# Optimization experiments

Hardware: AMD Instinct MI355X
Metric: run time of the kernel (lower is better)

## Reference

```python
import jax, jax.numpy as jnp
import numpy as np

N, E = 20000, 320000
IN_DIM, EDGE_DIM, HID = 64, 16, 64
# (in_c, heads, channels, out_c) per layer; last layer heads=1, concat=False
DIMS = [(64, 4, 64, 256), (256, 4, 64, 256), (256, 1, 64, 64)]


def _ln(x, g, b):
    m = x.mean(-1, keepdims=True)
    v = x.var(-1, keepdims=True)
    return (x - m) / jnp.sqrt(v + 1e-5) * g + b


def _gatv2(x, ei, ea, Wl, bl, Wr, br, We, att, bc, concat):
    # PyG GATv2Conv, eval mode (no dropout), add_self_loops=True, fill_value='mean'
    n = x.shape[0]
    H, C = att.shape
    ar = jnp.arange(n, dtype=ei.dtype)
    src = jnp.concatenate([ei[0], ar])
    dst = jnp.concatenate([ei[1], ar])
    ea_f = jnp.concatenate([ea, jnp.broadcast_to(ea.mean(0), (n, ea.shape[1]))], 0)
    xl = (x @ Wl + bl).reshape(n, H, C)   # source transform
    xr = (x @ Wr + br).reshape(n, H, C)   # target transform
    ee = (ea_f @ We).reshape(-1, H, C)    # edge transform (no bias in PyG)
    e = jax.nn.leaky_relu(xl[src] + xr[dst] + ee, 0.2)       # [E+N, H, C]
    score = jnp.einsum('ehc,hc->eh', e, att)                 # [E+N, H]
    mx = jax.ops.segment_max(score, dst, num_segments=n)
    a = jnp.exp(score - mx[dst])
    a = a / (jax.ops.segment_sum(a, dst, num_segments=n)[dst] + 1e-16)
    out = jax.ops.segment_sum(a[:, :, None] * xl[src], dst, num_segments=n)  # [N,H,C]
    out = out.reshape(n, H * C) if concat else out.mean(1)
    return out + bc


def _forward(x, eis, eas, Wp, bp, gp, bep, layers):
    h = jax.nn.gelu(_ln(x @ Wp + bp, gp, bep), approximate=False)
    for i in range(3):
        Wl, bl, Wr, br, We, att, bc, g, be, Wsk, bsk = layers[i]
        res = h @ Wsk + bsk
        h = _gatv2(h, eis[i], eas[i], Wl, bl, Wr, br, We, att, bc, i < 2)
        h = jax.nn.gelu(_ln(h, g, be), approximate=False) + res
    return h


def setup_inputs() -> dict:
    key = jax.random.key(0)
    ks = iter(jax.random.split(key, 64))
    rn = lambda shape, s=0.05: jax.random.normal(next(ks), shape, jnp.float32) * s
    d = {'x': jax.random.normal(next(ks), (N, IN_DIM), jnp.float32)}
    for i in range(3):
        d['ei%d' % i] = jax.random.randint(next(ks), (2, E), 0, N, jnp.int32)
        d['ea%d' % i] = jax.random.normal(next(ks), (E, EDGE_DIM), jnp.float32)
    d['Wp'] = rn((IN_DIM, HID)); d['bp'] = jnp.zeros(HID)
    d['gp'] = jnp.ones(HID); d['bep'] = jnp.zeros(HID)
    for i, (ic, H, C, oc) in enumerate(DIMS):
        hc = H * C
        d['Wl%d' % i] = rn((ic, hc)); d['bl%d' % i] = jnp.zeros(hc)
        d['Wr%d' % i] = rn((ic, hc)); d['br%d' % i] = jnp.zeros(hc)
        d['We%d' % i] = rn((EDGE_DIM, hc))
        d['att%d' % i] = rn((H, C), 0.1)
        d['bc%d' % i] = jnp.zeros(hc if i < 2 else C)
        d['g%d' % i] = jnp.ones(oc); d['be%d' % i] = jnp.zeros(oc)
        d['Wsk%d' % i] = rn((ic, oc)); d['bsk%d' % i] = jnp.zeros(oc)
    return d


def reference(x, ei0, ea0, ei1, ea1, ei2, ea2, Wp, bp, gp, bep,
              Wl0, bl0, Wr0, br0, We0, att0, bc0, g0, be0, Wsk0, bsk0,
              Wl1, bl1, Wr1, br1, We1, att1, bc1, g1, be1, Wsk1, bsk1,
              Wl2, bl2, Wr2, br2, We2, att2, bc2, g2, be2, Wsk2, bsk2):
    layers = [
        (Wl0, bl0, Wr0, br0, We0, att0, bc0, g0, be0, Wsk0, bsk0),
        (Wl1, bl1, Wr1, br1, We1, att1, bc1, g1, be1, Wsk1, bsk1),
        (Wl2, bl2, Wr2, br2, We2, att2, bc2, g2, be2, Wsk2, bsk2),
    ]
    return _forward(x, (ei0, ei1, ei2), (ea0, ea1, ea2), Wp, bp, gp, bep, layers)
```

## Files before the change

kernel.cpp:

```cpp
#include <hip/hip_runtime.h>
#include <hip/hip_bf16.h>
#include <math.h>

#define NV 20000
#define NE 320000
#define CSR_PAD 8

typedef __attribute__((ext_vector_type(8))) short bf16x8;
typedef __attribute__((ext_vector_type(4))) float f32x4;
typedef __attribute__((ext_vector_type(2))) _Float16 h2;

static __device__ __forceinline__ ushort f2b(float f) {
  __hip_bfloat16 h = __float2bfloat16(f);
  return *reinterpret_cast<ushort*>(&h);
}
static __device__ __forceinline__ float b2f(ushort u) {
  union { ushort s[2]; float f; } c;
  c.s[0] = 0; c.s[1] = u;
  return c.f;
}
static __device__ __forceinline__ ushort f2h(float f) {
  _Float16 h = (_Float16)f;
  return *reinterpret_cast<ushort*>(&h);
}
static __device__ __forceinline__ float blo(unsigned u) { return __uint_as_float(u << 16); }
static __device__ __forceinline__ float bhi(unsigned u) { return __uint_as_float(u & 0xffff0000u); }

static __device__ __forceinline__ float wave_sum64(float x) {
  x += __int_as_float(__builtin_amdgcn_update_dpp(0, __float_as_int(x), 0x111, 0xF, 0xF, true));
  x += __int_as_float(__builtin_amdgcn_update_dpp(0, __float_as_int(x), 0x112, 0xF, 0xF, true));
  x += __int_as_float(__builtin_amdgcn_update_dpp(0, __float_as_int(x), 0x114, 0xF, 0xF, true));
  x += __int_as_float(__builtin_amdgcn_update_dpp(0, __float_as_int(x), 0x118, 0xF, 0xF, true));
  x += __int_as_float(__builtin_amdgcn_update_dpp(0, __float_as_int(x), 0x142, 0xA, 0xF, true));
  x += __int_as_float(__builtin_amdgcn_update_dpp(0, __float_as_int(x), 0x143, 0xC, 0xF, true));
  return __int_as_float(__builtin_amdgcn_readlane(__float_as_int(x), 63));
}

static __device__ __forceinline__ float sum16(float x) {
  x += __int_as_float(__builtin_amdgcn_update_dpp(0, __float_as_int(x), 0x121, 0xF, 0xF, true));
  x += __int_as_float(__builtin_amdgcn_update_dpp(0, __float_as_int(x), 0x122, 0xF, 0xF, true));
  x += __int_as_float(__builtin_amdgcn_update_dpp(0, __float_as_int(x), 0x124, 0xF, 0xF, true));
  x += __int_as_float(__builtin_amdgcn_update_dpp(0, __float_as_int(x), 0x128, 0xF, 0xF, true));
  return x;
}

static __device__ __forceinline__ float dot16h(const uint4* __restrict__ E,
                                               const h2* __restrict__ Wch) {
#if __has_builtin(__builtin_amdgcn_fdot2)
  const h2* e = (const h2*)E;
  float s = 0.f;
#pragma unroll
  for (int j = 0; j < 8; ++j) s = __builtin_amdgcn_fdot2(e[j], Wch[j], s, false);
  return s;
#else
  const unsigned* u = (const unsigned*)E;
  float s = 0.f;
#pragma unroll
  for (int j = 0; j < 8; ++j) {
    union { unsigned v; h2 h; } cv; cv.v = u[j];
    s = fmaf((float)cv.h[0], (float)Wch[j][0], s);
    s = fmaf((float)cv.h[1], (float)Wch[j][1], s);
  }
  return s;
#endif
}

struct CJob { const float* src; ushort* dst; int K, M; };
struct PrepArgs {
  const int* ei[3];
  const float* ea[3];
  int* counts[3];
  float* easum[3];
  CJob jobs[9];
  const float *x, *Wp, *bp, *gp, *bep;
  ushort* h0;
};

__global__ __launch_bounds__(256) void prep_kernel(PrepArgs a) {
  const int y = blockIdx.y, t = threadIdx.x;
  if (y < 3) {
    if (blockIdx.x < 256) {
      const float4* ea4 = (const float4*)a.ea[y];
      const int cg = t & 3;
      int r = blockIdx.x * 64 + (t >> 2);
      const int rstride = 256 * 64;
      float4 s = make_float4(0.f, 0.f, 0.f, 0.f);
      for (; r < NE; r += rstride) {
        float4 v = ea4[(size_t)r * 4 + cg];
        s.x += v.x; s.y += v.y; s.z += v.z; s.w += v.w;
      }
      __shared__ float4 red4[256];
      red4[t] = s;
      __syncthreads();
      if (t < 4) {
        float4 tot = make_float4(0.f, 0.f, 0.f, 0.f);
        for (int j = t; j < 256; j += 4) {
          float4 v = red4[j];
          tot.x += v.x; tot.y += v.y; tot.z += v.z; tot.w += v.w;
        }
        atomicAdd(&a.easum[y][t * 4 + 0], tot.x);
        atomicAdd(&a.easum[y][t * 4 + 1], tot.y);
        atomicAdd(&a.easum[y][t * 4 + 2], tot.z);
        atomicAdd(&a.easum[y][t * 4 + 3], tot.w);
      }
    }
    int i = blockIdx.x * 256 + t;
    if (i < NE) atomicAdd(&a.counts[y][a.ei[y][NE + i]], 1);
  } else if (y == 3) {
#pragma unroll
    for (int j = 0; j < 9; ++j) {
      CJob jb = a.jobs[j];
      const int total = jb.M * jb.K;
      for (int i = blockIdx.x * 256 + t; i < total; i += gridDim.x * 256) {
        int m = i / jb.K, k = i - m * jb.K;
        jb.dst[i] = f2b(jb.src[(size_t)k * jb.M + m]);
      }
    }
  } else {
    int wid = t >> 6, lane = t & 63;
    for (int row = blockIdx.x * 4 + wid; row < NV; row += gridDim.x * 4) {
      float xv = a.x[(size_t)row * 64 + lane];
      float acc = a.bp[lane];
#pragma unroll
      for (int k = 0; k < 64; ++k) {
        float v = __shfl(xv, k, 64);
        acc = fmaf(v, a.Wp[k * 64 + lane], acc);
      }
      float s1 = wave_sum64(acc), s2 = wave_sum64(acc * acc);
      float mean = s1 * (1.0f / 64.0f);
      float var  = s2 * (1.0f / 64.0f) - mean * mean;
      float yv = (acc - mean) * rsqrtf(var + 1e-5f) * a.gp[lane] + a.bep[lane];
      float gel = 0.5f * yv * (1.0f + erff(yv * 0.70710678118654752f));
      a.h0[(size_t)row * 64 + lane] = f2b(gel);
    }
  }
}

__global__ __launch_bounds__(1024) void scan_kernel(
    int* __restrict__ countsA, int* __restrict__ cursorA)
{
  int* counts = countsA + blockIdx.x * (NV + 1);
  int* cursor = cursorA + blockIdx.x * NV;
  __shared__ int ws[16];
  __shared__ int wexcl[17];
  const int t = threadIdx.x, lane = t & 63, wid = t >> 6;
  const int base = t * 20;
  int v[20];
  int tot = 0;
#pragma unroll
  for (int j = 0; j < 20; ++j) {
    int i = base + j;
    v[j] = (i < NV) ? counts[i] : 0;
    tot += v[j];
  }
  int x = tot;
#pragma unroll
  for (int o = 1; o < 64; o <<= 1) {
    int yy = __shfl_up(x, o, 64);
    if (lane >= o) x += yy;
  }
  if (lane == 63) ws[wid] = x;
  __syncthreads();
  if (t == 0) {
    int r = 0;
#pragma unroll
    for (int j = 0; j < 16; ++j) { wexcl[j] = r; r += ws[j]; }
    wexcl[16] = r;
  }
  __syncthreads();
  int run = wexcl[wid] + (x - tot);
#pragma unroll
  for (int j = 0; j < 20; ++j) {
    int i = base + j;
    if (i < NV) { counts[i] = run; cursor[i] = run; }
    run += v[j];
  }
  if (t == 0) counts[NV] = wexcl[16];
}

struct G0SArgs {
  const ushort *A, *WT;
  const float *b0, *b1, *b2;
  ushort *O0, *O1; float* O2;
  int K, M1, M2, Mtot, NT;
  const int* ei[3]; const float* ea[3];
  int* cursor;
  unsigned* csr[3]; ushort* eab[3]; int HC[3];
};

__global__ __launch_bounds__(256) void gemm0_scatter_kernel(G0SArgs a) {
  __shared__ ushort As[128][40];
  __shared__ ushort Bs[64][40];
  const int t = threadIdx.x;
  if ((int)blockIdx.x < a.NT) {
    const int wave = t >> 6, lane = t & 63;
    const int mcols = a.Mtot >> 6;
    const int col0 = ((int)blockIdx.x % mcols) * 64, row0 = ((int)blockIdx.x / mcols) * 128;
    const int m_ = lane & 15, q = lane >> 4;
    f32x4 acc[2][4];
#pragma unroll
    for (int i = 0; i < 2; ++i)
#pragma unroll
      for (int j = 0; j < 4; ++j) acc[i][j] = (f32x4){0.f, 0.f, 0.f, 0.f};
    const int ar = t >> 1, ac = (t & 1) * 16;
    const int br = t >> 2, bcol = (t & 3) * 8;
    const ushort* Ap = a.A + (size_t)(row0 + ar) * a.K + ac;
    const ushort* Bp = a.WT + (size_t)(col0 + br) * a.K + bcol;
    const bool a_ok = (row0 + ar) < NV;
    for (int k0 = 0; k0 < a.K; k0 += 32) {
      uint4 av0 = make_uint4(0, 0, 0, 0), av1 = make_uint4(0, 0, 0, 0);
      if (a_ok) { av0 = *(const uint4*)(Ap + k0); av1 = *(const uint4*)(Ap + k0 + 8); }
      uint4 bv = *(const uint4*)(Bp + k0);
      *(uint4*)&As[ar][ac] = av0;
      *(uint4*)&As[ar][ac + 8] = av1;
      *(uint4*)&Bs[br][bcol] = bv;
      __syncthreads();
      bf16x8 a0 = *(const bf16x8*)&As[wave * 32 + m_][q * 8];
      bf16x8 a1 = *(const bf16x8*)&As[wave * 32 + 16 + m_][q * 8];
#pragma unroll
      for (int cf = 0; cf < 4; ++cf) {
        bf16x8 b = *(const bf16x8*)&Bs[cf * 16 + m_][q * 8];
        acc[0][cf] = __builtin_amdgcn_mfma_f32_16x16x32_bf16(a0, b, acc[0][cf], 0, 0, 0);
        acc[1][cf] = __builtin_amdgcn_mfma_f32_16x16x32_bf16(a1, b, acc[1][cf], 0, 0, 0);
      }
      __syncthreads();
    }
    const float* bias; int base, mode, Wd;
    if (col0 < a.M1)      { bias = a.b0; base = 0;    mode = 0; Wd = a.M1; }
    else if (col0 < a.M2) { bias = a.b1; base = a.M1; mode = 1; Wd = a.M2 - a.M1; }
    else                  { bias = a.b2; base = a.M2; mode = 2; Wd = a.Mtot - a.M2; }
#pragma unroll
    for (int rf = 0; rf < 2; ++rf) {
#pragma unroll
      for (int cf = 0; cf < 4; ++cf) {
        int col = col0 + cf * 16 + m_ - base;
        float bb = bias[col];
#pragma unroll
        for (int r = 0; r < 4; ++r) {
          int row = row0 + wave * 32 + rf * 16 + q * 4 + r;
          if (row < NV) {
            float v = acc[rf][cf][r] + bb;
            if (mode == 0)      a.O0[(size_t)row * Wd + col] = f2b(v);
            else if (mode == 1) a.O1[(size_t)row * Wd + col] = f2b(v);
            else                a.O2[(size_t)row * Wd + col] = v;
          }
        }
      }
    }
  } else {
    const int per = NE + CSR_PAD;
    int gi = ((int)blockIdx.x - a.NT) * 256 + t;
    if (gi >= 3 * per) return;
    int l = gi / per, i = gi - l * per;
    if (i >= NE) {
      a.csr[l][i] = 0u;
      uint4 z = make_uint4(0, 0, 0, 0);
      *(uint4*)(a.eab[l] + (size_t)i * 16) = z;
      *(uint4*)(a.eab[l] + (size_t)i * 16 + 8) = z;
      return;
    }
    int dst = a.ei[l][NE + i], src = a.ei[l][i];
    int pos = atomicAdd(&a.cursor[(size_t)l * NV + dst], 1);
    a.csr[l][pos] = (unsigned)(src * a.HC[l]);
    const float4* er = (const float4*)(a.ea[l] + (size_t)i * 16);
    float4 q0 = er[0], q1 = er[1], q2 = er[2], q3 = er[3];
    uint4 w0, w1;
    w0.x = (unsigned)f2h(q0.x) | ((unsigned)f2h(q0.y) << 16);
    w0.y = (unsigned)f2h(q0.z) | ((unsigned)f2h(q0.w) << 16);
    w0.z = (unsigned)f2h(q1.x) | ((unsigned)f2h(q1.y) << 16);
    w0.w = (unsigned)f2h(q1.z) | ((unsigned)f2h(q1.w) << 16);
    w1.x = (unsigned)f2h(q2.x) | ((unsigned)f2h(q2.y) << 16);
    w1.y = (unsigned)f2h(q2.z) | ((unsigned)f2h(q2.w) << 16);
    w1.z = (unsigned)f2h(q3.x) | ((unsigned)f2h(q3.y) << 16);
    w1.w = (unsigned)f2h(q3.z) | ((unsigned)f2h(q3.w) << 16);
    *(uint4*)(a.eab[l] + (size_t)pos * 16) = w0;
    *(uint4*)(a.eab[l] + (size_t)pos * 16 + 8) = w1;
  }
}

__global__ __launch_bounds__(256) void gemm_fused(
    const ushort* __restrict__ A, const ushort* __restrict__ WT,
    const float* __restrict__ b0, const float* __restrict__ b1,
    const float* __restrict__ b2,
    ushort* __restrict__ O0, ushort* __restrict__ O1, float* __restrict__ O2,
    int N, int K, int M1, int M2, int Mtot)
{
  __shared__ ushort As[128][40];
  __shared__ ushort Bs[64][40];
  const int t = threadIdx.x, wave = t >> 6, lane = t & 63;
  const int row0 = blockIdx.y * 128, col0 = blockIdx.x * 64;
  const int m_ = lane & 15, q = lane >> 4;
  f32x4 acc[2][4];
#pragma unroll
  for (int i = 0; i < 2; ++i)
#pragma unroll
    for (int j = 0; j < 4; ++j) acc[i][j] = (f32x4){0.f, 0.f, 0.f, 0.f};
  const int ar = t >> 1, ac = (t & 1) * 16;
  const int br = t >> 2, bcol = (t & 3) * 8;
  const ushort* Ap = A + (size_t)(row0 + ar) * K + ac;
  const ushort* Bp = WT + (size_t)(col0 + br) * K + bcol;
  const bool a_ok = (row0 + ar) < N;
  for (int k0 = 0; k0 < K; k0 += 32) {
    uint4 av0 = make_uint4(0, 0, 0, 0), av1 = make_uint4(0, 0, 0, 0);
    if (a_ok) { av0 = *(const uint4*)(Ap + k0); av1 = *(const uint4*)(Ap + k0 + 8); }
    uint4 bv = *(const uint4*)(Bp + k0);
    *(uint4*)&As[ar][ac] = av0;
    *(uint4*)&As[ar][ac + 8] = av1;
    *(uint4*)&Bs[br][bcol] = bv;
    __syncthreads();
    bf16x8 a0 = *(const bf16x8*)&As[wave * 32 + m_][q * 8];
    bf16x8 a1 = *(const bf16x8*)&As[wave * 32 + 16 + m_][q * 8];
#pragma unroll
    for (int cf = 0; cf < 4; ++cf) {
      bf16x8 b = *(const bf16x8*)&Bs[cf * 16 + m_][q * 8];
      acc[0][cf] = __builtin_amdgcn_mfma_f32_16x16x32_bf16(a0, b, acc[0][cf], 0, 0, 0);
      acc[1][cf] = __builtin_amdgcn_mfma_f32_16x16x32_bf16(a1, b, acc[1][cf], 0, 0, 0);
    }
    __syncthreads();
  }
  const float* bias; int base, mode, Wd;
  if (col0 < M1)      { bias = b0; base = 0;  mode = 0; Wd = M1; }
  else if (col0 < M2) { bias = b1; base = M1; mode = 1; Wd = M2 - M1; }
  else                { bias = b2; base = M2; mode = 2; Wd = Mtot - M2; }
#pragma unroll
  for (int rf = 0; rf < 2; ++rf) {
#pragma unroll
    for (int cf = 0; cf < 4; ++cf) {
      int col = col0 + cf * 16 + m_ - base;
      float bb = bias[col];
#pragma unroll
      for (int r = 0; r < 4; ++r) {
        int row = row0 + wave * 32 + rf * 16 + q * 4 + r;
        if (row < N) {
          float v = acc[rf][cf][r] + bb;
          if (mode == 0)      O0[(size_t)row * Wd + col] = f2b(v);
          else if (mode == 1) O1[(size_t)row * Wd + col] = f2b(v);
          else                O2[(size_t)row * Wd + col] = v;
        }
      }
    }
  }
}

__global__ __launch_bounds__(256) void agg4_kernel(
    const ushort* __restrict__ eab, const float* __restrict__ easum,
    const float* __restrict__ We,
    const ushort* __restrict__ xl, const ushort* __restrict__ xr,
    const float* __restrict__ att, const float* __restrict__ bc,
    const float* __restrict__ g, const float* __restrict__ be,
    const float* __restrict__ res,
    const int* __restrict__ offs, const unsigned* __restrict__ csr,
    ushort* __restrict__ houtb, int E)
{
  const int t = threadIdx.x, lane = t & 63, wave = t >> 6;
  const int n = blockIdx.x * 4 + wave;
  const int cb = 4 * lane;
  const size_t rowb = (size_t)n * 256 + cb;
  const float L2E = 1.4426950408889634f;

  float4 atv = *(const float4*)(att + cb);
  float at[4] = {atv.x * L2E, atv.y * L2E, atv.z * L2E, atv.w * L2E};

  h2 Wch[4][8];
  float esf[4] = {0.f, 0.f, 0.f, 0.f};
#pragma unroll
  for (int k = 0; k < 8; ++k) {
    float4 wr0 = *(const float4*)(We + (2 * k) * 256 + cb);
    float4 wr1 = *(const float4*)(We + (2 * k + 1) * 256 + cb);
    const float* w0 = &wr0.x;
    const float* w1 = &wr1.x;
    float e0 = easum[2 * k], e1 = easum[2 * k + 1];
#pragma unroll
    for (int j = 0; j < 4; ++j) {
      esf[j] = fmaf(e0, w0[j], esf[j]);
      esf[j] = fmaf(e1, w1[j], esf[j]);
      Wch[j][k] = (h2){(_Float16)w0[j], (_Float16)w1[j]};
    }
  }
#pragma unroll
  for (int j = 0; j < 4; ++j) esf[j] *= 1.0f / (float)E;

  uint2 qr = *(const uint2*)(xr + rowb);
  float xrv[4] = {blo(qr.x), bhi(qr.x), blo(qr.y), bhi(qr.y)};
  uint2 qn = *(const uint2*)(xl + rowb);
  float xln[4] = {blo(qn.x), bhi(qn.x), blo(qn.y), bhi(qn.y)};

  float p = 0.f;
#pragma unroll
  for (int j = 0; j < 4; ++j) {
    float v = xln[j] + xrv[j] + esf[j];
    v = v > 0.f ? v : 0.2f * v;
    p = fmaf(v, at[j], p);
  }
  float wself = exp2f(sum16(p));
  float acc[4];
#pragma unroll
  for (int j = 0; j < 4; ++j) acc[j] = wself * xln[j];
  float denom = wself;

  const int beg = __builtin_amdgcn_readfirstlane(offs[n]);
  const int end = __builtin_amdgcn_readfirstlane(offs[n + 1]);

  unsigned P[2];
  uint4 EA[2][2];
  uint2 XL[2];
#pragma unroll
  for (int k = 0; k < 2; ++k) {
    P[k] = csr[beg + k];
    const uint4* ep = (const uint4*)(eab + (size_t)(beg + k) * 16);
    EA[k][0] = ep[0]; EA[k][1] = ep[1];
  }
#pragma unroll
  for (int k = 0; k < 2; ++k)
    XL[k] = *(const uint2*)(xl + __builtin_amdgcn_readfirstlane(P[k]) + cb);

  for (int idx = beg; idx < end; idx += 2) {
    unsigned Q[2];
    uint4 EB[2][2];
    uint2 XN[2];
#pragma unroll
    for (int k = 0; k < 2; ++k) Q[k] = csr[idx + 2 + k];
#pragma unroll
    for (int k = 0; k < 2; ++k) {
      const uint4* ep = (const uint4*)(eab + (size_t)(idx + 2 + k) * 16);
      EB[k][0] = ep[0]; EB[k][1] = ep[1];
    }
#pragma unroll
    for (int k = 0; k < 2; ++k)
      XN[k] = *(const uint2*)(xl + __builtin_amdgcn_readfirstlane(Q[k]) + cb);

#pragma unroll
    for (int k = 0; k < 2; ++k) {
      float xf[4] = {blo(XL[k].x), bhi(XL[k].x), blo(XL[k].y), bhi(XL[k].y)};
      float pp = 0.f;
#pragma unroll
      for (int j = 0; j < 4; ++j) {
        float ee = dot16h(EA[k], Wch[j]);
        float v = xf[j] + xrv[j] + ee;
        v = v > 0.f ? v : 0.2f * v;
        pp = fmaf(v, at[j], pp);
      }
      float S = sum16(pp);
      float w = (idx + k < end) ? exp2f(S) : 0.f;
#pragma unroll
      for (int j = 0; j < 4; ++j) acc[j] = fmaf(w, xf[j], acc[j]);
      denom += w;
    }
#pragma unroll
    for (int k = 0; k < 2; ++k) { P[k] = Q[k]; EA[k][0] = EB[k][0]; EA[k][1] = EB[k][1]; XL[k] = XN[k]; }
  }

  const float inv = 1.0f / (denom + 1e-16f);
  float4 bcv = *(const float4*)(bc + cb);
  float out[4];
  out[0] = acc[0] * inv + bcv.x; out[1] = acc[1] * inv + bcv.y;
  out[2] = acc[2] * inv + bcv.z; out[3] = acc[3] * inv + bcv.w;

  float so1 = out[0] + out[1] + out[2] + out[3];
  float so2 = out[0] * out[0] + out[1] * out[1] + out[2] * out[2] + out[3] * out[3];
  float s1 = wave_sum64(so1), s2 = wave_sum64(so2);
  float mean = s1 * (1.0f / 256.0f);
  float var  = s2 * (1.0f / 256.0f) - mean * mean;
  float rstd = rsqrtf(var + 1e-5f);
  float4 gv = *(const float4*)(g + cb);
  float4 bev = *(const float4*)(be + cb);
  float4 rv = *(const float4*)(res + rowb);
  const float* gp = &gv.x; const float* bep = &bev.x; const float* rp = &rv.x;
  ushort ob[4];
#pragma unroll
  for (int j = 0; j < 4; ++j) {
    float y = (out[j] - mean) * rstd * gp[j] + bep[j];
    float gel = 0.5f * y * (1.0f + erff(y * 0.70710678118654752f));
    ob[j] = f2b(gel + rp[j]);
  }
  uint2 ov;
  ov.x = (unsigned)ob[0] | ((unsigned)ob[1] << 16);
  ov.y = (unsigned)ob[2] | ((unsigned)ob[3] << 16);
  *(uint2*)(houtb + rowb) = ov;
}

__global__ __launch_bounds__(256, 4) void agg1_kernel(
    const ushort* __restrict__ eab, const float* __restrict__ easum,
    const float* __restrict__ We,
    const ushort* __restrict__ xl, const ushort* __restrict__ xr,
    const float* __restrict__ att, const float* __restrict__ bc,
    const float* __restrict__ g, const float* __restrict__ be,
    const float* __restrict__ res,
    const int* __restrict__ offs, const unsigned* __restrict__ csr,
    float* __restrict__ houtf, int E)
{
  const int HC = 64;
  const int t = threadIdx.x, lane = t & 63, wave = t >> 6;
  const int n = blockIdx.x * 4 + wave;
  const int c = lane;

  const float xr_t = b2f(xr[(size_t)n * HC + c]);
  const float att_t = att[c] * 1.4426950408889634f;
  float eself = 0.f;
  h2 Wch[8];
#pragma unroll
  for (int j = 0; j < 8; ++j) {
    float w0 = We[(2 * j) * HC + c], w1 = We[(2 * j + 1) * HC + c];
    eself = fmaf(easum[2 * j], w0, eself);
    eself = fmaf(easum[2 * j + 1], w1, eself);
    Wch[j] = (h2){(_Float16)w0, (_Float16)w1};
  }
  eself *= 1.0f / (float)E;

  const float xln = b2f(xl[(size_t)n * HC + c]);
  float vs = xln + xr_t + eself;
  vs = vs > 0.f ? vs : 0.2f * vs;
  const float wself = exp2f(wave_sum64(vs * att_t));
  float acc = wself * xln, denom = wself;

  const int beg = __builtin_amdgcn_readfirstlane(offs[n]);
  const int end = __builtin_amdgcn_readfirstlane(offs[n + 1]);

  unsigned P[4];
  uint4 EA[4][2];
  float XL[4];
#pragma unroll
  for (int k = 0; k < 4; ++k) {
    P[k] = csr[beg + k];
    const uint4* ep = (const uint4*)(eab + (size_t)(beg + k) * 16);
    EA[k][0] = ep[0]; EA[k][1] = ep[1];
  }
#pragma unroll
  for (int k = 0; k < 4; ++k)
    XL[k] = b2f(xl[__builtin_amdgcn_readfirstlane(P[k]) + c]);

  for (int idx = beg; idx < end; idx += 4) {
    unsigned Q[4];
    uint4 EB[4][2];
    float XLN[4];
#pragma unroll
    for (int k = 0; k < 4; ++k) Q[k] = csr[idx + 4 + k];
#pragma unroll
    for (int k = 0; k < 4; ++k) {
      const uint4* ep = (const uint4*)(eab + (size_t)(idx + 4 + k) * 16);
      EB[k][0] = ep[0]; EB[k][1] = ep[1];
    }
#pragma unroll
    for (int k = 0; k < 4; ++k)
      XLN[k] = b2f(xl[__builtin_amdgcn_readfirstlane(Q[k]) + c]);

    float wv[4];
#pragma unroll
    for (int k = 0; k < 4; ++k) {
      float ee = dot16h(EA[k], Wch);
      float v = XL[k] + xr_t + ee;
      v = v > 0.f ? v : 0.2f * v;
      float S = wave_sum64(v * att_t);
      wv[k] = (idx + k < end) ? exp2f(S) : 0.f;
    }
#pragma unroll
    for (int k = 0; k < 4; ++k) { acc = fmaf(wv[k], XL[k], acc); denom += wv[k]; }
#pragma unroll
    for (int k = 0; k < 4; ++k) {
      P[k] = Q[k]; EA[k][0] = EB[k][0]; EA[k][1] = EB[k][1]; XL[k] = XLN[k];
    }
  }

  float out = acc / (denom + 1e-16f) + bc[c];
  float s1 = wave_sum64(out), s2 = wave_sum64(out * out);
  float mean = s1 / (float)HC;
  float var  = s2 / (float)HC - mean * mean;
  float y = (out - mean) * rsqrtf(var + 1e-5f) * g[c] + be[c];
  float gel = 0.5f * y * (1.0f + erff(y * 0.70710678118654752f));
  houtf[(size_t)n * HC + c] = gel + res[(size_t)n * HC + c];
}

extern "C" void kernel_launch(void* const* d_in, const int* in_sizes, int n_in,
                              void* d_out, int out_size, void* d_ws, size_t ws_size,
                              hipStream_t stream)
{
  auto in = [&](int i) { return (const float*)d_in[i]; };

  const int ic[3] = {64, 256, 256}, hc[3] = {256, 256, 64}, oc[3] = {256, 256, 64};
  const int CSRN = NE + CSR_PAD;

  char* w = (char*)d_ws;
  size_t off = 0;
  auto alloc = [&](size_t bytes) { void* p = w + off; off = (off + bytes + 511) & ~(size_t)511; return p; };
  ushort* B1   = (ushort*)alloc((size_t)NV * 256 * 2);
  ushort* B2   = (ushort*)alloc((size_t)NV * 256 * 2);
  float*  B3   = (float*)alloc((size_t)NV * 256 * 4);
  ushort* h0bf = (ushort*)alloc((size_t)NV * 64 * 2);
  ushort* h1bf = (ushort*)alloc((size_t)NV * 256 * 2);
  ushort* h2bf = (ushort*)alloc((size_t)NV * 256 * 2);
  ushort* Wcat[3];
  for (int i = 0; i < 3; ++i)
    Wcat[i] = (ushort*)alloc((size_t)(2 * hc[i] + oc[i]) * ic[i] * 2);
  float*    easumA  = (float*)alloc(3 * 64);
  int*      countsA = (int*)alloc((size_t)3 * (NV + 1) * 4);
  int*      cursorA = (int*)alloc((size_t)3 * NV * 4);
  unsigned* csrA    = (unsigned*)alloc((size_t)3 * CSRN * 4);
  ushort*   eabA    = (ushort*)alloc((size_t)3 * CSRN * 16 * 2);

  hipMemsetAsync(easumA, 0, 512 + (size_t)3 * (NV + 1) * 4, stream);

  PrepArgs pa;
  for (int i = 0; i < 3; ++i) {
    pa.ei[i] = (const int*)d_in[1 + 2 * i];
    pa.ea[i] = in(2 + 2 * i);
    pa.counts[i] = countsA + i * (NV + 1);
    pa.easum[i] = easumA + i * 16;
    pa.jobs[i * 3 + 0] = {in(11 + 11 * i), Wcat[i],                             ic[i], hc[i]};
    pa.jobs[i * 3 + 1] = {in(13 + 11 * i), Wcat[i] + (size_t)hc[i] * ic[i],     ic[i], hc[i]};
    pa.jobs[i * 3 + 2] = {in(20 + 11 * i), Wcat[i] + (size_t)2 * hc[i] * ic[i], ic[i], oc[i]};
  }
  pa.x = in(0); pa.Wp = in(7); pa.bp = in(8); pa.gp = in(9); pa.bep = in(10);
  pa.h0 = h0bf;
  prep_kernel<<<dim3(1344, 5), 256, 0, stream>>>(pa);

  scan_kernel<<<3, 1024, 0, stream>>>(countsA, cursorA);

  G0SArgs ga;
  ga.A = h0bf; ga.WT = Wcat[0];
  ga.b0 = in(12); ga.b1 = in(14); ga.b2 = in(21);
  ga.O0 = B1; ga.O1 = B2; ga.O2 = B3;
  ga.K = 64; ga.M1 = 256; ga.M2 = 512; ga.Mtot = 768;
  ga.NT = (768 / 64) * ((NV + 127) / 128);
  for (int i = 0; i < 3; ++i) {
    ga.ei[i] = (const int*)d_in[1 + 2 * i];
    ga.ea[i] = in(2 + 2 * i);
    ga.csr[i] = csrA + (size_t)i * CSRN;
    ga.eab[i] = eabA + (size_t)i * CSRN * 16;
    ga.HC[i] = hc[i];
  }
  ga.cursor = cursorA;
  const int scat_blocks = (3 * (NE + CSR_PAD) + 255) / 256;
  gemm0_scatter_kernel<<<ga.NT + scat_blocks, 256, 0, stream>>>(ga);

  agg4_kernel<<<NV / 4, 256, 0, stream>>>(
      eabA + 0, easumA + 0, in(15), B1, B2, in(16), in(17), in(18), in(19),
      B3, countsA, csrA, h1bf, NE);

  gemm_fused<<<dim3(768 / 64, (NV + 127) / 128), 256, 0, stream>>>(
      h1bf, Wcat[1], in(23), in(25), in(32), B1, B2, B3, NV, 256, 256, 512, 768);

  agg4_kernel<<<NV / 4, 256, 0, stream>>>(
      eabA + (size_t)CSRN * 16, easumA + 16, in(26), B1, B2, in(27), in(28),
      in(29), in(30), B3, countsA + (NV + 1), csrA + (size_t)CSRN, h2bf, NE);

  gemm_fused<<<dim3(192 / 64, (NV + 127) / 128), 256, 0, stream>>>(
      h2bf, Wcat[2], in(34), in(36), in(43), B1, B2, B3, NV, 256, 64, 128, 192);

  agg1_kernel<<<NV / 4, 256, 0, stream>>>(
      eabA + (size_t)2 * CSRN * 16, easumA + 32, in(37), B1, B2, in(38), in(39),
      in(40), in(41), B3, countsA + 2 * (NV + 1), csrA + (size_t)2 * CSRN,
      (float*)d_out, NE);
}
```

Before: 538.7 us.

## Store edge attrs in original order and index them via CSR pairs

The fp16 conversion of edge attributes moves into the prep kernel, which already streams the edge attributes for the mean. It writes them in original edge order instead of scattering them into CSR order. The CSR entries become (source offset, edge-attr offset) pairs, so the scatter pass writes 8 bytes per edge instead of 36. The aggregation kernels then gather edge attributes indirectly, in random order, instead of reading them sequentially, which trades coalesced reads in three aggregation passes for a cheaper build step. Padding entries point to edge 0, whose weight is masked anyway.

```diff
diff --git a/kernel.cpp b/kernel.cpp
--- a/kernel.cpp
+++ b/kernel.cpp
@@ -71,6 +71,7 @@
   const float* ea[3];
   int* counts[3];
   float* easum[3];
+  ushort* eab[3];
   CJob jobs[9];
   const float *x, *Wp, *bp, *gp, *bep;
   ushort* h0;
@@ -81,6 +82,7 @@
   if (y < 3) {
     if (blockIdx.x < 256) {
       const float4* ea4 = (const float4*)a.ea[y];
+      ushort* eab = a.eab[y];
       const int cg = t & 3;
       int r = blockIdx.x * 64 + (t >> 2);
       const int rstride = 256 * 64;
@@ -88,6 +90,10 @@
       for (; r < NE; r += rstride) {
         float4 v = ea4[(size_t)r * 4 + cg];
         s.x += v.x; s.y += v.y; s.z += v.z; s.w += v.w;
+        uint2 pk;
+        pk.x = (unsigned)f2h(v.x) | ((unsigned)f2h(v.y) << 16);
+        pk.y = (unsigned)f2h(v.z) | ((unsigned)f2h(v.w) << 16);
+        *(uint2*)(eab + (size_t)r * 16 + cg * 4) = pk;
       }
       __shared__ float4 red4[256];
       red4[t] = s;
@@ -183,9 +189,9 @@
   const float *b0, *b1, *b2;
   ushort *O0, *O1; float* O2;
   int K, M1, M2, Mtot, NT;
-  const int* ei[3]; const float* ea[3];
+  const int* ei[3];
   int* cursor;
-  unsigned* csr[3]; ushort* eab[3]; int HC[3];
+  uint2* csr2[3]; int HC[3];
 };
 
 __global__ __launch_bounds__(256) void gemm0_scatter_kernel(G0SArgs a) {
@@ -252,29 +258,10 @@
     int gi = ((int)blockIdx.x - a.NT) * 256 + t;
     if (gi >= 3 * per) return;
     int l = gi / per, i = gi - l * per;
-    if (i >= NE) {
-      a.csr[l][i] = 0u;
-      uint4 z = make_uint4(0, 0, 0, 0);
-      *(uint4*)(a.eab[l] + (size_t)i * 16) = z;
-      *(uint4*)(a.eab[l] + (size_t)i * 16 + 8) = z;
-      return;
-    }
+    if (i >= NE) { a.csr2[l][i] = make_uint2(0u, 0u); return; }
     int dst = a.ei[l][NE + i], src = a.ei[l][i];
     int pos = atomicAdd(&a.cursor[(size_t)l * NV + dst], 1);
-    a.csr[l][pos] = (unsigned)(src * a.HC[l]);
-    const float4* er = (const float4*)(a.ea[l] + (size_t)i * 16);
-    float4 q0 = er[0], q1 = er[1], q2 = er[2], q3 = er[3];
-    uint4 w0, w1;
-    w0.x = (unsigned)f2h(q0.x) | ((unsigned)f2h(q0.y) << 16);
-    w0.y = (unsigned)f2h(q0.z) | ((unsigned)f2h(q0.w) << 16);
-    w0.z = (unsigned)f2h(q1.x) | ((unsigned)f2h(q1.y) << 16);
-    w0.w = (unsigned)f2h(q1.z) | ((unsigned)f2h(q1.w) << 16);
-    w1.x = (unsigned)f2h(q2.x) | ((unsigned)f2h(q2.y) << 16);
-    w1.y = (unsigned)f2h(q2.z) | ((unsigned)f2h(q2.w) << 16);
-    w1.z = (unsigned)f2h(q3.x) | ((unsigned)f2h(q3.y) << 16);
-    w1.w = (unsigned)f2h(q3.z) | ((unsigned)f2h(q3.w) << 16);
-    *(uint4*)(a.eab[l] + (size_t)pos * 16) = w0;
-    *(uint4*)(a.eab[l] + (size_t)pos * 16 + 8) = w1;
+    a.csr2[l][pos] = make_uint2((unsigned)(src * a.HC[l]), (unsigned)(i * 16));
   }
 }
 
@@ -349,7 +336,7 @@
     const float* __restrict__ att, const float* __restrict__ bc,
     const float* __restrict__ g, const float* __restrict__ be,
     const float* __restrict__ res,
-    const int* __restrict__ offs, const unsigned* __restrict__ csr,
+    const int* __restrict__ offs, const uint2* __restrict__ csr2,
     ushort* __restrict__ houtb, int E)
 {
   const int t = threadIdx.x, lane = t & 63, wave = t >> 6;
@@ -401,33 +388,32 @@
   const int beg = __builtin_amdgcn_readfirstlane(offs[n]);
   const int end = __builtin_amdgcn_readfirstlane(offs[n + 1]);
 
-  unsigned P[2];
+  uint2 P[2];
   uint4 EA[2][2];
   uint2 XL[2];
 #pragma unroll
+  for (int k = 0; k < 2; ++k) P[k] = csr2[beg + k];
+#pragma unroll
   for (int k = 0; k < 2; ++k) {
-    P[k] = csr[beg + k];
-    const uint4* ep = (const uint4*)(eab + (size_t)(beg + k) * 16);
+    const unsigned eo = __builtin_amdgcn_readfirstlane(P[k].y);
+    const uint4* ep = (const uint4*)(eab + eo);
     EA[k][0] = ep[0]; EA[k][1] = ep[1];
-  }
-#pragma unroll
-  for (int k = 0; k < 2; ++k)
-    XL[k] = *(const uint2*)(xl + __builtin_amdgcn_readfirstlane(P[k]) + cb);
+    XL[k] = *(const uint2*)(xl + __builtin_amdgcn_readfirstlane(P[k].x) + cb);
+  }
 
   for (int idx = beg; idx < end; idx += 2) {
-    unsigned Q[2];
+    uint2 Q[2];
     uint4 EB[2][2];
     uint2 XN[2];
 #pragma unroll
-    for (int k = 0; k < 2; ++k) Q[k] = csr[idx + 2 + k];
+    for (int k = 0; k < 2; ++k) Q[k] = csr2[idx + 2 + k];
 #pragma unroll
     for (int k = 0; k < 2; ++k) {
-      const uint4* ep = (const uint4*)(eab + (size_t)(idx + 2 + k) * 16);
+      const unsigned eo = __builtin_amdgcn_readfirstlane(Q[k].y);
+      const uint4* ep = (const uint4*)(eab + eo);
       EB[k][0] = ep[0]; EB[k][1] = ep[1];
-    }
-#pragma unroll
-    for (int k = 0; k < 2; ++k)
-      XN[k] = *(const uint2*)(xl + __builtin_amdgcn_readfirstlane(Q[k]) + cb);
+      XN[k] = *(const uint2*)(xl + __builtin_amdgcn_readfirstlane(Q[k].x) + cb);
+    }
 
 #pragma unroll
     for (int k = 0; k < 2; ++k) {
@@ -486,7 +472,7 @@
     const float* __restrict__ att, const float* __restrict__ bc,
     const float* __restrict__ g, const float* __restrict__ be,
     const float* __restrict__ res,
-    const int* __restrict__ offs, const unsigned* __restrict__ csr,
+    const int* __restrict__ offs, const uint2* __restrict__ csr2,
     float* __restrict__ houtf, int E)
 {
   const int HC = 64;
@@ -516,33 +502,32 @@
   const int beg = __builtin_amdgcn_readfirstlane(offs[n]);
   const int end = __builtin_amdgcn_readfirstlane(offs[n + 1]);
 
-  unsigned P[4];
+  uint2 P[4];
   uint4 EA[4][2];
   float XL[4];
 #pragma unroll
+  for (int k = 0; k < 4; ++k) P[k] = csr2[beg + k];
+#pragma unroll
   for (int k = 0; k < 4; ++k) {
-    P[k] = csr[beg + k];
-    const uint4* ep = (const uint4*)(eab + (size_t)(beg + k) * 16);
+    const unsigned eo = __builtin_amdgcn_readfirstlane(P[k].y);
+    const uint4* ep = (const uint4*)(eab + eo);
     EA[k][0] = ep[0]; EA[k][1] = ep[1];
-  }
-#pragma unroll
-  for (int k = 0; k < 4; ++k)
-    XL[k] = b2f(xl[__builtin_amdgcn_readfirstlane(P[k]) + c]);
+    XL[k] = b2f(xl[__builtin_amdgcn_readfirstlane(P[k].x) + c]);
+  }
 
   for (int idx = beg; idx < end; idx += 4) {
-    unsigned Q[4];
+    uint2 Q[4];
     uint4 EB[4][2];
     float XLN[4];
 #pragma unroll
-    for (int k = 0; k < 4; ++k) Q[k] = csr[idx + 4 + k];
+    for (int k = 0; k < 4; ++k) Q[k] = csr2[idx + 4 + k];
 #pragma unroll
     for (int k = 0; k < 4; ++k) {
-      const uint4* ep = (const uint4*)(eab + (size_t)(idx + 4 + k) * 16);
+      const unsigned eo = __builtin_amdgcn_readfirstlane(Q[k].y);
+      const uint4* ep = (const uint4*)(eab + eo);
       EB[k][0] = ep[0]; EB[k][1] = ep[1];
-    }
-#pragma unroll
-    for (int k = 0; k < 4; ++k)
-      XLN[k] = b2f(xl[__builtin_amdgcn_readfirstlane(Q[k]) + c]);
+      XLN[k] = b2f(xl[__builtin_amdgcn_readfirstlane(Q[k].x) + c]);
+    }
 
     float wv[4];
 #pragma unroll
@@ -591,11 +576,11 @@
   ushort* Wcat[3];
   for (int i = 0; i < 3; ++i)
     Wcat[i] = (ushort*)alloc((size_t)(2 * hc[i] + oc[i]) * ic[i] * 2);
-  float*    easumA  = (float*)alloc(3 * 64);
-  int*      countsA = (int*)alloc((size_t)3 * (NV + 1) * 4);
-  int*      cursorA = (int*)alloc((size_t)3 * NV * 4);
-  unsigned* csrA    = (unsigned*)alloc((size_t)3 * CSRN * 4);
-  ushort*   eabA    = (ushort*)alloc((size_t)3 * CSRN * 16 * 2);
+  float*  easumA  = (float*)alloc(3 * 64);
+  int*    countsA = (int*)alloc((size_t)3 * (NV + 1) * 4);
+  int*    cursorA = (int*)alloc((size_t)3 * NV * 4);
+  uint2*  csr2A   = (uint2*)alloc((size_t)3 * CSRN * 8);
+  ushort* eabA    = (ushort*)alloc((size_t)3 * CSRN * 16 * 2);
 
   hipMemsetAsync(easumA, 0, 512 + (size_t)3 * (NV + 1) * 4, stream);
 
@@ -605,6 +590,7 @@
     pa.ea[i] = in(2 + 2 * i);
     pa.counts[i] = countsA + i * (NV + 1);
     pa.easum[i] = easumA + i * 16;
+    pa.eab[i] = eabA + (size_t)i * CSRN * 16;
     pa.jobs[i * 3 + 0] = {in(11 + 11 * i), Wcat[i],                             ic[i], hc[i]};
     pa.jobs[i * 3 + 1] = {in(13 + 11 * i), Wcat[i] + (size_t)hc[i] * ic[i],     ic[i], hc[i]};
     pa.jobs[i * 3 + 2] = {in(20 + 11 * i), Wcat[i] + (size_t)2 * hc[i] * ic[i], ic[i], oc[i]};
@@ -623,9 +609,7 @@
   ga.NT = (768 / 64) * ((NV + 127) / 128);
   for (int i = 0; i < 3; ++i) {
     ga.ei[i] = (const int*)d_in[1 + 2 * i];
-    ga.ea[i] = in(2 + 2 * i);
-    ga.csr[i] = csrA + (size_t)i * CSRN;
-    ga.eab[i] = eabA + (size_t)i * CSRN * 16;
+    ga.csr2[i] = csr2A + (size_t)i * CSRN;
     ga.HC[i] = hc[i];
   }
   ga.cursor = cursorA;
@@ -634,20 +618,20 @@
 
   agg4_kernel<<<NV / 4, 256, 0, stream>>>(
       eabA + 0, easumA + 0, in(15), B1, B2, in(16), in(17), in(18), in(19),
-      B3, countsA, csrA, h1bf, NE);
+      B3, countsA, csr2A, h1bf, NE);
 
   gemm_fused<<<dim3(768 / 64, (NV + 127) / 128), 256, 0, stream>>>(
       h1bf, Wcat[1], in(23), in(25), in(32), B1, B2, B3, NV, 256, 256, 512, 768);
 
   agg4_kernel<<<NV / 4, 256, 0, stream>>>(
       eabA + (size_t)CSRN * 16, easumA + 16, in(26), B1, B2, in(27), in(28),
-      in(29), in(30), B3, countsA + (NV + 1), csrA + (size_t)CSRN, h2bf, NE);
+      in(29), in(30), B3, countsA + (NV + 1), csr2A + (size_t)CSRN, h2bf, NE);
 
   gemm_fused<<<dim3(192 / 64, (NV + 127) / 128), 256, 0, stream>>>(
       h2bf, Wcat[2], in(34), in(36), in(43), B1, B2, B3, NV, 256, 64, 128, 192);
 
   agg1_kernel<<<NV / 4, 256, 0, stream>>>(
       eabA + (size_t)2 * CSRN * 16, easumA + 32, in(37), B1, B2, in(38), in(39),
-      in(40), in(41), B3, countsA + 2 * (NV + 1), csrA + (size_t)2 * CSRN,
+      in(40), in(41), B3, countsA + 2 * (NV + 1), csr2A + (size_t)2 * CSRN,
       (float*)d_out, NE);
 }
```

New measurement: 567.7 us. 5.4% more time.
